# Performance work log

Measured on AMD Instinct MI355X. Metric: run time of the kernel, lower is better.

The kernel has to match this reference:

```python
import jax, jax.numpy as jnp
import numpy as np

B, C, Dz, Hh, Ww = 1, 128, 24, 24, 24
L = Dz * Hh * Ww
D_STATE = 16
D_CONV = 4
EXPAND = 2
D_INNER = EXPAND * C
DT_RANK = (C + 15) // 16  # ceil(d_model/16) = 8


def setup_inputs() -> dict:
    key = jax.random.key(0)
    ks = jax.random.split(key, 10)
    s = 0.02
    return {
        "x": jax.random.normal(ks[0], (B, C, Dz, Hh, Ww), dtype=jnp.float32),
        "ln_w": jnp.ones((C,), jnp.float32),
        "ln_b": jnp.zeros((C,), jnp.float32),
        "in_proj_w": s * jax.random.normal(ks[1], (2 * D_INNER, C), jnp.float32),
        "conv_w": s * jax.random.normal(ks[2], (D_INNER, D_CONV), jnp.float32),
        "conv_b": jnp.zeros((D_INNER,), jnp.float32),
        "x_proj_w": s * jax.random.normal(ks[3], (DT_RANK + 2 * D_STATE, D_INNER), jnp.float32),
        "dt_proj_w": s * jax.random.normal(ks[4], (D_INNER, DT_RANK), jnp.float32),
        "dt_proj_b": jax.random.uniform(ks[5], (D_INNER,), jnp.float32, -4.0, -2.0),
        "A_log": jnp.log(jnp.broadcast_to(jnp.arange(1, D_STATE + 1, dtype=jnp.float32), (D_INNER, D_STATE))),
        "D_param": jnp.ones((D_INNER,), jnp.float32),
        "out_proj_w": s * jax.random.normal(ks[6], (C, D_INNER), jnp.float32),
    }


def _mamba_forward(x, ln_w, ln_b, in_proj_w, conv_w, conv_b, x_proj_w,
                   dt_proj_w, dt_proj_b, A_log, D_param, out_proj_w):
    b, c, d, h, w = x.shape
    l = d * h * w
    tokens = x.reshape(b, c, l).transpose(0, 2, 1)  # (B,L,C)

    # LayerNorm over channel dim
    mu = jnp.mean(tokens, axis=-1, keepdims=True)
    var = jnp.var(tokens, axis=-1, keepdims=True)
    tn = (tokens - mu) * jax.lax.rsqrt(var + 1e-5) * ln_w + ln_b

    # in_proj -> x, z
    xz = jnp.einsum('blc,ec->ble', tn, in_proj_w)  # (B,L,2*d_inner)
    xs, z = jnp.split(xz, 2, axis=-1)

    # causal depthwise conv1d over L (kernel size D_CONV)
    xpad = jnp.pad(xs, ((0, 0), (D_CONV - 1, 0), (0, 0)))
    xc = conv_b
    xc = sum(xpad[:, k:k + l, :] * conv_w[:, k] for k in range(D_CONV)) + conv_b
    xa = jax.nn.silu(xc)  # (B,L,d_inner)

    # x_proj -> dt, B, C
    x_dbl = jnp.einsum('bld,ed->ble', xa, x_proj_w)
    dt_in = x_dbl[..., :DT_RANK]
    Bm = x_dbl[..., DT_RANK:DT_RANK + D_STATE]          # (B,L,d_state)
    Cm = x_dbl[..., DT_RANK + D_STATE:]                 # (B,L,d_state)
    dt = jax.nn.softplus(jnp.einsum('blr,dr->bld', dt_in, dt_proj_w) + dt_proj_b)

    A = -jnp.exp(A_log)  # (d_inner, d_state)

    def step(hst, inp):
        dt_t, B_t, C_t, x_t = inp  # (B,d_inner),(B,d_state),(B,d_state),(B,d_inner)
        dA = jnp.exp(dt_t[..., None] * A)                       # (B,d_inner,d_state)
        hst = dA * hst + (dt_t * x_t)[..., None] * B_t[:, None, :]
        y_t = jnp.einsum('bds,bs->bd', hst, C_t)
        return hst, y_t

    h0 = jnp.zeros((b, D_INNER, D_STATE), xa.dtype)
    xs_t = (dt.transpose(1, 0, 2), Bm.transpose(1, 0, 2), Cm.transpose(1, 0, 2), xa.transpose(1, 0, 2))
    _, ys = jax.lax.scan(step, h0, xs_t)
    y = ys.transpose(1, 0, 2) + xa * D_param  # (B,L,d_inner)

    y = y * jax.nn.silu(z)
    out = jnp.einsum('bld,cd->blc', y, out_proj_w)

    tokens = tokens + out
    return tokens.transpose(0, 2, 1).reshape(b, c, d, h, w)


def reference(x, ln_w, ln_b, in_proj_w, conv_w, conv_b, x_proj_w,
              dt_proj_w, dt_proj_b, A_log, D_param, out_proj_w):
    return _mamba_forward(x, ln_w, ln_b, in_proj_w, conv_w, conv_b, x_proj_w,
                          dt_proj_w, dt_proj_b, A_log, D_param, out_proj_w)
```

## Files before the change

kernel.cpp:

```cpp
#include <hip/hip_runtime.h>
#include <hip/hip_bf16.h>
#include <math.h>


constexpr int LQ = 13824;
constexpr int NC = 216;
constexpr int CH = 64;
constexpr int NB = 108;
constexpr int DI = 256;
constexpr int DS = 16;

typedef __attribute__((ext_vector_type(8))) short short8v;
typedef __attribute__((ext_vector_type(4))) float float4v;

__device__ __forceinline__ ushort f2bf(float f) {
  uint u = __float_as_uint(f);
  u += 0x7FFFu + ((u >> 16) & 1u);
  return (ushort)(u >> 16);
}
__device__ __forceinline__ float bf2f(ushort u) {
  return __uint_as_float(((uint)u) << 16);
}
__device__ __forceinline__ void gl_lds16(const ushort* g, ushort* l) {
  __builtin_amdgcn_global_load_lds(
      (const __attribute__((address_space(1))) void*)g,
      (__attribute__((address_space(3))) void*)l, 16, 0, 0);
}

template<int CTRL>
__device__ __forceinline__ float dpp_add(float x) {
  int y = __builtin_amdgcn_update_dpp(0, __float_as_int(x), CTRL, 0xF, 0xF, true);
  return x + __int_as_float(y);
}
__device__ __forceinline__ float quad_reduce(float t) {
  t = dpp_add<0xB1>(t);
  t = dpp_add<0x4E>(t);
  return t;
}
__device__ __forceinline__ float softplus_f(float x) {
  return (x > 20.f) ? x : log1pf(__expf(x));
}

__global__ __launch_bounds__(256) void prep_w2(const float* __restrict__ w_in,
    const float* __restrict__ w_xp, const float* __restrict__ w_dt,
    const float* __restrict__ w_out,
    ushort* __restrict__ b_in, ushort* __restrict__ b_xp2, ushort* __restrict__ b_out) {
  int idx = blockIdx.x * 256 + threadIdx.x;
  if (idx < 65536) {
    b_in[idx] = f2bf(w_in[idx]);
  } else if (idx < 65536 + 8192) {
    int j = idx - 65536; int r = j >> 8, k = j & 255;
    b_xp2[j] = f2bf(w_xp[(8 + r) * 256 + k]);
  } else if (idx < 65536 + 8192 + 65536) {
    int j = idx - (65536 + 8192); int d = j >> 8, k = j & 255;
    float acc = 0.f;
    #pragma unroll
    for (int r = 0; r < 8; ++r) acc += w_dt[d * 8 + r] * w_xp[r * 256 + k];
    b_xp2[8192 + j] = f2bf(acc);
  } else if (idx < 65536 + 8192 + 65536 + 8192) {
    b_xp2[73728 + (idx - 139264)] = 0;
  } else if (idx < 180224) {
    int j = idx - 147456;
    b_out[j] = f2bf(w_out[j]);
  }
}

__global__ __launch_bounds__(256) void ln_t(const float* __restrict__ x,
    const float* __restrict__ lnw, const float* __restrict__ lnb,
    ushort* __restrict__ tn) {
  __shared__ float red[64][8];
  __shared__ float stat[64][2];
  __shared__ ushort T[64][136];
  const int t = threadIdx.x;
  const int l = t & 63, q = t >> 6;
  const int l0 = blockIdx.x * 64;
  float sum = 0.f, sq = 0.f;
  #pragma unroll 8
  for (int cc = 0; cc < 32; ++cc) {
    int c = q * 32 + cc;
    float v = x[(size_t)c * LQ + l0 + l];
    sum += v; sq += v * v;
  }
  red[l][q] = sum; red[l][4 + q] = sq;
  __syncthreads();
  if (t < 64) {
    float s  = red[t][0] + red[t][1] + red[t][2] + red[t][3];
    float s2 = red[t][4] + red[t][5] + red[t][6] + red[t][7];
    float mu = s * (1.f / 128.f);
    float var = s2 * (1.f / 128.f) - mu * mu;
    stat[t][0] = mu; stat[t][1] = rsqrtf(var + 1e-5f);
  }
  __syncthreads();
  float mu = stat[l][0], rs = stat[l][1];
  #pragma unroll 8
  for (int cc = 0; cc < 32; ++cc) {
    int c = q * 32 + cc;
    float v = x[(size_t)c * LQ + l0 + l];
    T[l][c] = f2bf((v - mu) * rs * lnw[c] + lnb[c]);
  }
  __syncthreads();
  int row = t >> 2, seg = t & 3;
  #pragma unroll
  for (int j = 0; j < 4; ++j) {
    short8v v = *(const short8v*)&T[row][seg * 32 + j * 8];
    *(short8v*)&tn[(size_t)(l0 + row) * 128 + seg * 32 + j * 8] = v;
  }
}

template<int K, int MV, int BSTR, int CSTR>
__global__ __launch_bounds__(256) void gemm_tok(
    const ushort* __restrict__ Wb,
    const ushort* __restrict__ Act,
    ushort* __restrict__ Out) {
  constexpr int KO = K / 8;
  __shared__ ushort As[64 * K];
  __shared__ ushort Bs[2][128 * 64];
  const int tid = threadIdx.x;
  const int l0 = blockIdx.x * 128;
  const int m0 = blockIdx.y * 64;
  #pragma unroll
  for (int i = 0; i < (64 * KO) / 256; ++i) {
    int cid = i * 256 + tid;
    int m = cid / KO, oct = cid % KO;
    short8v v = *(const short8v*)&Wb[(size_t)(m0 + m) * K + oct * 8];
    *(short8v*)&As[m * K + ((oct ^ (m & 7)) * 8)] = v;
  }
  #pragma unroll
  for (int i = 0; i < 4; ++i) {
    int cid = i * 256 + tid;
    int l = cid >> 3, oct = (cid & 7) ^ (l & 7);
    gl_lds16(&Act[(size_t)(l0 + l) * BSTR + oct * 8], &Bs[0][cid * 8]);
  }
  float4v acc[4][2];
  #pragma unroll
  for (int a = 0; a < 4; ++a)
    #pragma unroll
    for (int b = 0; b < 2; ++b) acc[a][b] = (float4v)0.f;
  const int w = tid >> 6, lane = tid & 63;
  const int r = lane & 15, g = lane >> 4;
  int buf = 0;
  __syncthreads();
  for (int k0 = 0; k0 < K; k0 += 64) {
    if (k0 + 64 < K) {
      #pragma unroll
      for (int i = 0; i < 4; ++i) {
        int cid = i * 256 + tid;
        int l = cid >> 3, oct = (cid & 7) ^ (l & 7);
        gl_lds16(&Act[(size_t)(l0 + l) * BSTR + (k0 + 64) + oct * 8],
                 &Bs[buf ^ 1][cid * 8]);
      }
    }
    const ushort* bp = Bs[buf];
    #pragma unroll
    for (int kk = 0; kk < 2; ++kk) {
      short8v af[4], bfv[2];
      int ko = (k0 >> 3) + kk * 4 + g;
      #pragma unroll
      for (int mf = 0; mf < 4; ++mf) {
        int row = mf * 16 + r;
        af[mf] = *(const short8v*)&As[row * K + ((ko ^ (row & 7)) * 8)];
      }
      int kob = kk * 4 + g;
      #pragma unroll
      for (int nf = 0; nf < 2; ++nf) {
        int row = w * 32 + nf * 16 + r;
        bfv[nf] = *(const short8v*)&bp[row * 64 + ((kob ^ (row & 7)) * 8)];
      }
      #pragma unroll
      for (int mf = 0; mf < 4; ++mf)
        #pragma unroll
        for (int nf = 0; nf < 2; ++nf)
          acc[mf][nf] = __builtin_amdgcn_mfma_f32_16x16x32_bf16(af[mf], bfv[nf], acc[mf][nf], 0, 0, 0);
    }
    __syncthreads();
    buf ^= 1;
  }
  #pragma unroll
  for (int mf = 0; mf < 4; ++mf) {
    #pragma unroll
    for (int nf = 0; nf < 2; ++nf) {
      int l = w * 32 + nf * 16 + r;
      int m = mf * 16 + g * 4;
      ushort u0 = f2bf(acc[mf][nf][0]), u1 = f2bf(acc[mf][nf][1]);
      ushort u2 = f2bf(acc[mf][nf][2]), u3 = f2bf(acc[mf][nf][3]);
      uint2 pk = make_uint2((uint)u0 | ((uint)u1 << 16), (uint)u2 | ((uint)u3 << 16));
      int oct = (m >> 3) ^ (l & 7);
      *(uint2*)&Bs[0][l * 64 + oct * 8 + (g & 1) * 4] = pk;
    }
  }
  __syncthreads();
  #pragma unroll
  for (int i = 0; i < 4; ++i) {
    int cid = i * 256 + tid;
    int row = cid >> 3, oct = cid & 7;
    if (oct * 8 < MV) {
      short8v v = *(const short8v*)&Bs[0][row * 64 + ((oct ^ (row & 7)) * 8)];
      *(short8v*)&Out[(size_t)(l0 + row) * CSTR + m0 + oct * 8] = v;
    }
  }
}

__global__ __launch_bounds__(256) void gemm_out_k(
    const ushort* __restrict__ Wb,
    const ushort* __restrict__ Yg,
    const float* __restrict__ X,
    float* __restrict__ Out) {
  __shared__ ushort Ay[2][128 * 64];
  __shared__ ushort Bw[64 * 256];
  const int tid = threadIdx.x;
  const int l0 = blockIdx.x * 128;
  const int c0 = blockIdx.y * 64;
  const int w = tid >> 6, lane = tid & 63;
  const int r = lane & 15, g = lane >> 4;
  #pragma unroll
  for (int i = 0; i < 8; ++i) {
    int cid = i * 256 + tid;
    int row = cid >> 5, oct = cid & 31;
    short8v vb = *(const short8v*)&Wb[(size_t)(c0 + row) * 256 + oct * 8];
    *(short8v*)&Bw[row * 256 + ((oct ^ (row & 7)) * 8)] = vb;
  }
  #pragma unroll
  for (int i = 0; i < 4; ++i) {
    int cid = i * 256 + tid;
    int row = cid >> 3, oct = (cid & 7) ^ (row & 7);
    gl_lds16(&Yg[((size_t)(oct >> 1) * LQ + l0 + row) * 16 + (oct & 1) * 8],
             &Ay[0][cid * 8]);
  }
  float4v acc[2][4];
  #pragma unroll
  for (int a = 0; a < 2; ++a)
    #pragma unroll
    for (int b = 0; b < 4; ++b) acc[a][b] = (float4v)0.f;
  int buf = 0;
  __syncthreads();
  for (int k0 = 0; k0 < 256; k0 += 64) {
    if (k0 + 64 < 256) {
      int ks = (k0 + 64) >> 4;
      #pragma unroll
      for (int i = 0; i < 4; ++i) {
        int cid = i * 256 + tid;
        int row = cid >> 3, oct = (cid & 7) ^ (row & 7);
        gl_lds16(&Yg[((size_t)(ks + (oct >> 1)) * LQ + l0 + row) * 16 + (oct & 1) * 8],
                 &Ay[buf ^ 1][cid * 8]);
      }
    }
    const ushort* ap = Ay[buf];
    #pragma unroll
    for (int kk = 0; kk < 2; ++kk) {
      int kob = kk * 4 + g;
      int ko = (k0 >> 3) + kob;
      short8v af[2], bfv[4];
      #pragma unroll
      for (int mf = 0; mf < 2; ++mf) {
        int row = w * 32 + mf * 16 + r;
        af[mf] = *(const short8v*)&ap[row * 64 + ((kob ^ (row & 7)) * 8)];
      }
      #pragma unroll
      for (int nf = 0; nf < 4; ++nf) {
        int row = nf * 16 + r;
        bfv[nf] = *(const short8v*)&Bw[row * 256 + ((ko ^ (row & 7)) * 8)];
      }
      #pragma unroll
      for (int mf = 0; mf < 2; ++mf)
        #pragma unroll
        for (int nf = 0; nf < 4; ++nf)
          acc[mf][nf] = __builtin_amdgcn_mfma_f32_16x16x32_bf16(af[mf], bfv[nf], acc[mf][nf], 0, 0, 0);
    }
    __syncthreads();
    buf ^= 1;
  }
  #pragma unroll
  for (int mf = 0; mf < 2; ++mf) {
    #pragma unroll
    for (int nf = 0; nf < 4; ++nf) {
      int c = c0 + nf * 16 + r;
      int l = l0 + w * 32 + mf * 16 + g * 4;
      size_t off = (size_t)c * LQ + l;
      float4 rv = *(const float4*)&X[off];
      float4 o = make_float4(acc[mf][nf][0] + rv.x, acc[mf][nf][1] + rv.y,
                             acc[mf][nf][2] + rv.z, acc[mf][nf][3] + rv.w);
      *(float4*)&Out[off] = o;
    }
  }
}

__global__ __launch_bounds__(256) void conv2(const ushort* __restrict__ xz,
    const float* __restrict__ cw, const float* __restrict__ cb,
    ushort* __restrict__ xa) {
  const int tid = threadIdx.x;
  const int d0 = (tid & 31) * 8;
  const int l0 = blockIdx.x * 32 + (tid >> 5) * 4;
  float w0[8], w1[8], w2[8], w3[8], bb[8];
  #pragma unroll
  for (int j = 0; j < 8; ++j) {
    float4 wv = *(const float4*)&cw[(d0 + j) * 4];
    w0[j] = wv.x; w1[j] = wv.y; w2[j] = wv.z; w3[j] = wv.w;
    bb[j] = cb[d0 + j];
  }
  float rbuf[7][8];
  #pragma unroll
  for (int t = 0; t < 7; ++t) {
    int ls = l0 - 3 + t;
    if (ls >= 0) {
      short8v v = *(const short8v*)&xz[(size_t)ls * 512 + d0];
      #pragma unroll
      for (int j = 0; j < 8; ++j) rbuf[t][j] = bf2f((ushort)v[j]);
    } else {
      #pragma unroll
      for (int j = 0; j < 8; ++j) rbuf[t][j] = 0.f;
    }
  }
  #pragma unroll
  for (int i = 0; i < 4; ++i) {
    short8v ov;
    #pragma unroll
    for (int j = 0; j < 8; ++j) {
      float acc = bb[j] + w0[j] * rbuf[i][j] + w1[j] * rbuf[i + 1][j]
                        + w2[j] * rbuf[i + 2][j] + w3[j] * rbuf[i + 3][j];
      ov[j] = (short)f2bf(acc / (1.f + __expf(-acc)));
    }
    *(short8v*)&xa[(size_t)(l0 + i) * 256 + d0] = ov;
  }
}

__global__ __launch_bounds__(256) void scan1(const ushort* __restrict__ xdbl,
    const ushort* __restrict__ xa, const float* __restrict__ bias,
    const float* __restrict__ A_log, float* __restrict__ Stot, float* __restrict__ Hc,
    ushort* __restrict__ yloc) {
  __shared__ uint  duL[64 * 64];
  __shared__ float bcL[64 * 32];
  __shared__ ushort ylds[64 * 72];
  const int tid = threadIdx.x;
  const int c = blockIdx.x, dg = blockIdx.y;
  const int dloc = tid >> 2, sq = tid & 3;
  const int d = dg * 64 + dloc;
  const int lb = c * CH;
  float4v A, h;
  #pragma unroll
  for (int k = 0; k < 4; ++k) {
    A[k] = -__expf(A_log[d * 16 + sq * 4 + k]);
    h[k] = 0.f;
  }
  float S = 0.f;
  {
    const int doff = dg * 64 + sq * 16;
    const ushort* xr = xdbl + (size_t)(lb + dloc) * 320 + 32 + doff;
    const ushort* xar = xa + (size_t)(lb + dloc) * 256 + doff;
    short8v d0 = *(const short8v*)xr;
    short8v d1 = *(const short8v*)(xr + 8);
    short8v x0 = *(const short8v*)xar;
    short8v x1 = *(const short8v*)(xar + 8);
    uint pk[16];
    #pragma unroll
    for (int j = 0; j < 8; ++j) {
      float sp = softplus_f(bf2f((ushort)d0[j]) + bias[doff + j]);
      pk[j] = (uint)f2bf(sp) | ((uint)f2bf(sp * bf2f((ushort)x0[j])) << 16);
      float sp2 = softplus_f(bf2f((ushort)d1[j]) + bias[doff + 8 + j]);
      pk[8 + j] = (uint)f2bf(sp2) | ((uint)f2bf(sp2 * bf2f((ushort)x1[j])) << 16);
    }
    uint4* dst = (uint4*)&duL[dloc * 64 + sq * 16];
    #pragma unroll
    for (int j = 0; j < 4; ++j)
      dst[j] = make_uint4(pk[4 * j], pk[4 * j + 1], pk[4 * j + 2], pk[4 * j + 3]);
  }
  if (tid < 128) {
    int row = tid >> 1, half = tid & 1;
    const ushort* xr = xdbl + (size_t)(lb + row) * 320;
    short8v bv = *(const short8v*)(xr + half * 8);
    short8v cv = *(const short8v*)(xr + 16 + half * 8);
    float* bd = &bcL[row * 32 + half * 8];
    float* cd = &bcL[row * 32 + 16 + half * 8];
    #pragma unroll
    for (int j = 0; j < 8; ++j) {
      bd[j] = bf2f((ushort)bv[j]);
      cd[j] = bf2f((ushort)cv[j]);
    }
  }
  __syncthreads();
  #pragma unroll 4
  for (int i = 0; i < CH; ++i) {
    uint pv = duL[i * 64 + dloc];
    float dtv = __uint_as_float(pv << 16);
    float dxv = __uint_as_float(pv & 0xffff0000u);
    S += dtv;
    float4v Bv = *(const float4v*)&bcL[i * 32 + sq * 4];
    float4v Cv = *(const float4v*)&bcL[i * 32 + 16 + sq * 4];
    float t = 0.f;
    #pragma unroll
    for (int k = 0; k < 4; ++k) {
      float a = __expf(dtv * A[k]);
      h[k] = fmaf(a, h[k], dxv * Bv[k]);
      t = fmaf(h[k], Cv[k], t);
    }
    t = quad_reduce(t);
    if (sq == 0) ylds[i * 72 + dloc] = f2bf(t);
  }
  __syncthreads();
  {
    int slab = tid >> 6, row = tid & 63;
    short8v v0 = *(const short8v*)&ylds[row * 72 + slab * 16];
    short8v v1 = *(const short8v*)&ylds[row * 72 + slab * 16 + 8];
    ushort* dst = &yloc[((size_t)(dg * 4 + slab) * LQ + lb + row) * 16];
    *(short8v*)dst = v0;
    *(short8v*)(dst + 8) = v1;
  }
  *(float4*)&Hc[(size_t)(c * 256 + d) * 16 + sq * 4] = make_float4(h[0], h[1], h[2], h[3]);
  if (sq == 0) Stot[c * 256 + d] = S;
}

__global__ __launch_bounds__(256) void scan_combine(const float* __restrict__ Stot,
    const float* __restrict__ Hc, const float* __restrict__ A_log,
    float* __restrict__ Hin) {
  int t = blockIdx.x * 256 + threadIdx.x;
  int d = t >> 4;
  float A = -__expf(A_log[t]);
  float h = 0.f;
  for (int cb = 0; cb < NC; cb += 8) {
    float a[8], b[8];
    #pragma unroll
    for (int j = 0; j < 8; ++j) {
      a[j] = Stot[(cb + j) * 256 + d];
      b[j] = Hc[(size_t)(cb + j) * 4096 + t];
    }
    #pragma unroll
    for (int j = 0; j < 8; ++j) {
      Hin[(size_t)(cb + j) * 4096 + t] = h;
      h = fmaf(__expf(A * a[j]), h, b[j]);
    }
  }
}

__global__ __launch_bounds__(256) void scan2(const ushort* __restrict__ xdbl,
    const ushort* __restrict__ xa, const ushort* __restrict__ xz,
    const float* __restrict__ bias, const float* __restrict__ A_log,
    const float* __restrict__ Dp, const float* __restrict__ Hin,
    ushort* __restrict__ yg) {
  __shared__ uint  dtp[32 * 64];
  __shared__ float cL[64 * 16];
  __shared__ float corr[64 * 68];
  const int tid = threadIdx.x;
  const int c = blockIdx.x, dg = blockIdx.y;
  const int dloc = tid >> 2, sq = tid & 3;
  const int d = dg * 64 + dloc;
  const int lb = c * CH;
  float4v A, hin;
  #pragma unroll
  for (int k = 0; k < 4; ++k) A[k] = -__expf(A_log[d * 16 + sq * 4 + k]);
  {
    float4 hv = *(const float4*)&Hin[(size_t)(c * 256 + d) * 16 + sq * 4];
    hin[0] = hv.x; hin[1] = hv.y; hin[2] = hv.z; hin[3] = hv.w;
  }
  float S = 0.f;
  {
    int rp = tid >> 3, seg = tid & 7;
    const int doff = dg * 64 + seg * 8;
    const ushort* xr0 = xdbl + (size_t)(lb + 2 * rp) * 320 + 32 + doff;
    short8v e0 = *(const short8v*)xr0;
    short8v e1 = *(const short8v*)(xr0 + 320);
    uint pk[8];
    #pragma unroll
    for (int j = 0; j < 8; ++j) {
      float spe = softplus_f(bf2f((ushort)e0[j]) + bias[doff + j]);
      float spo = softplus_f(bf2f((ushort)e1[j]) + bias[doff + j]);
      pk[j] = (uint)f2bf(spe) | ((uint)f2bf(spo) << 16);
    }
    uint4* dst = (uint4*)&dtp[rp * 64 + seg * 8];
    dst[0] = make_uint4(pk[0], pk[1], pk[2], pk[3]);
    dst[1] = make_uint4(pk[4], pk[5], pk[6], pk[7]);
  }
  if (tid < 128) {
    int row = tid >> 1, half = tid & 1;
    short8v cv = *(const short8v*)(xdbl + (size_t)(lb + row) * 320 + 16 + half * 8);
    float* cd = &cL[row * 16 + half * 8];
    #pragma unroll
    for (int j = 0; j < 8; ++j) cd[j] = bf2f((ushort)cv[j]);
  }
  __syncthreads();
  #pragma unroll 2
  for (int i2 = 0; i2 < CH / 2; ++i2) {
    uint pv = dtp[i2 * 64 + dloc];
    #pragma unroll
    for (int par = 0; par < 2; ++par) {
      float dtv = (par == 0) ? __uint_as_float(pv << 16)
                             : __uint_as_float(pv & 0xffff0000u);
      S += dtv;
      int i = i2 * 2 + par;
      float4v Cv = *(const float4v*)&cL[i * 16 + sq * 4];
      float t = 0.f;
      #pragma unroll
      for (int k = 0; k < 4; ++k)
        t = fmaf(__expf(A[k] * S), hin[k] * Cv[k], t);
      t = quad_reduce(t);
      if (sq == 0) corr[i * 68 + dloc] = t;
    }
  }
  __syncthreads();
  {
    int slab = tid >> 6, row = tid & 63;
    const int doff = dg * 64 + slab * 16;
    size_t sl = ((size_t)(dg * 4 + slab) * LQ + lb + row) * 16;
    short8v y0 = *(const short8v*)&yg[sl];
    short8v y1 = *(const short8v*)&yg[sl + 8];
    const ushort* xav = xa + (size_t)(lb + row) * 256 + doff;
    short8v x0 = *(const short8v*)xav;
    short8v x1 = *(const short8v*)(xav + 8);
    const ushort* zvp = xz + (size_t)(lb + row) * 512 + 256 + doff;
    short8v z0 = *(const short8v*)zvp;
    short8v z1 = *(const short8v*)(zvp + 8);
    float4 c0 = *(const float4*)&corr[row * 68 + slab * 16];
    float4 c1 = *(const float4*)&corr[row * 68 + slab * 16 + 4];
    float4 c2 = *(const float4*)&corr[row * 68 + slab * 16 + 8];
    float4 c3 = *(const float4*)&corr[row * 68 + slab * 16 + 12];
    float cr[16] = {c0.x, c0.y, c0.z, c0.w, c1.x, c1.y, c1.z, c1.w,
                    c2.x, c2.y, c2.z, c2.w, c3.x, c3.y, c3.z, c3.w};
    short8v o0, o1;
    #pragma unroll
    for (int j = 0; j < 8; ++j) {
      float v0 = bf2f((ushort)y0[j]) + cr[j] + bf2f((ushort)x0[j]) * Dp[doff + j];
      float zf0 = bf2f((ushort)z0[j]);
      o0[j] = (short)f2bf(v0 * (zf0 / (1.f + __expf(-zf0))));
      float v1 = bf2f((ushort)y1[j]) + cr[8 + j] + bf2f((ushort)x1[j]) * Dp[doff + 8 + j];
      float zf1 = bf2f((ushort)z1[j]);
      o1[j] = (short)f2bf(v1 * (zf1 / (1.f + __expf(-zf1))));
    }
    *(short8v*)&yg[sl] = o0;
    *(short8v*)&yg[sl + 8] = o1;
  }
}

extern "C" void kernel_launch(void* const* d_in, const int* in_sizes, int n_in,
                              void* d_out, int out_size, void* d_ws, size_t ws_size,
                              hipStream_t stream) {
  const float* x         = (const float*)d_in[0];
  const float* ln_w      = (const float*)d_in[1];
  const float* ln_b      = (const float*)d_in[2];
  const float* in_proj_w = (const float*)d_in[3];
  const float* conv_w    = (const float*)d_in[4];
  const float* conv_b    = (const float*)d_in[5];
  const float* x_proj_w  = (const float*)d_in[6];
  const float* dt_proj_w = (const float*)d_in[7];
  const float* dt_proj_b = (const float*)d_in[8];
  const float* A_log     = (const float*)d_in[9];
  const float* D_param   = (const float*)d_in[10];
  const float* out_proj_w= (const float*)d_in[11];
  float* out = (float*)d_out;

  char* ws = (char*)d_ws;
  ushort* wbf_in  = (ushort*)(ws + 0);
  ushort* wbf_xp2 = (ushort*)(ws + 131072);
  ushort* wbf_out = (ushort*)(ws + 294912);
  float*  Hin     = (float*)(ws + 360448);
  float*  Hc      = (float*)(ws + 3899392);
  float*  Stot    = (float*)(ws + 7438336);
  ushort* tn_t    = (ushort*)(ws + 7659520);
  ushort* xz_t    = (ushort*)(ws + 11198464);
  ushort* xa_t    = (ushort*)(ws + 25354240);
  ushort* xdbl_t  = (ushort*)(ws + 32432128);
  ushort* yg_t    = (ushort*)(ws + 41279488);

  prep_w2<<<704, 256, 0, stream>>>(in_proj_w, x_proj_w, dt_proj_w, out_proj_w,
                                   wbf_in, wbf_xp2, wbf_out);
  ln_t<<<LQ / 64, 256, 0, stream>>>(x, ln_w, ln_b, tn_t);
  gemm_tok<128, 64, 128, 512><<<dim3(NB, 8), 256, 0, stream>>>(wbf_in, tn_t, xz_t);
  conv2<<<LQ / 32, 256, 0, stream>>>(xz_t, conv_w, conv_b, xa_t);
  gemm_tok<256, 64, 256, 320><<<dim3(NB, 5), 256, 0, stream>>>(wbf_xp2, xa_t, xdbl_t);
  scan1<<<dim3(NC, 4), 256, 0, stream>>>(xdbl_t, xa_t, dt_proj_b, A_log, Stot, Hc, yg_t);
  scan_combine<<<16, 256, 0, stream>>>(Stot, Hc, A_log, Hin);
  scan2<<<dim3(NC, 4), 256, 0, stream>>>(xdbl_t, xa_t, xz_t, dt_proj_b, A_log,
                                         D_param, Hin, yg_t);
  gemm_out_k<<<dim3(NB, 2), 256, 0, stream>>>(wbf_out, yg_t, x, out);
}
```

Measured before the change: 201.2 us.

## Fuse chunked scan stages into one cooperative kernel with grid syncs

```diff
diff --git a/kernel.cpp b/kernel.cpp
--- a/kernel.cpp
+++ b/kernel.cpp
@@ -1,6 +1,9 @@
 #include <hip/hip_runtime.h>
 #include <hip/hip_bf16.h>
+#include <hip/hip_cooperative_groups.h>
 #include <math.h>
+
+namespace cg = cooperative_groups;
 
 
 constexpr int LQ = 13824;
@@ -74,11 +77,12 @@
   const int t = threadIdx.x;
   const int l = t & 63, q = t >> 6;
   const int l0 = blockIdx.x * 64;
+  float vals[32];
   float sum = 0.f, sq = 0.f;
   #pragma unroll 8
   for (int cc = 0; cc < 32; ++cc) {
-    int c = q * 32 + cc;
-    float v = x[(size_t)c * LQ + l0 + l];
+    float v = x[(size_t)(q * 32 + cc) * LQ + l0 + l];
+    vals[cc] = v;
     sum += v; sq += v * v;
   }
   red[l][q] = sum; red[l][4 + q] = sq;
@@ -95,8 +99,7 @@
   #pragma unroll 8
   for (int cc = 0; cc < 32; ++cc) {
     int c = q * 32 + cc;
-    float v = x[(size_t)c * LQ + l0 + l];
-    T[l][c] = f2bf((v - mu) * rs * lnw[c] + lnb[c]);
+    T[l][c] = f2bf((vals[cc] - mu) * rs * lnw[c] + lnb[c]);
   }
   __syncthreads();
   int row = t >> 2, seg = t & 3;
@@ -323,13 +326,15 @@
   }
 }
 
-__global__ __launch_bounds__(256) void scan1(const ushort* __restrict__ xdbl,
-    const ushort* __restrict__ xa, const float* __restrict__ bias,
-    const float* __restrict__ A_log, float* __restrict__ Stot, float* __restrict__ Hc,
-    ushort* __restrict__ yloc) {
+__global__ __launch_bounds__(256, 4) void scan_fused(const ushort* __restrict__ xdbl,
+    const ushort* __restrict__ xa, const ushort* __restrict__ xz,
+    const float* __restrict__ bias, const float* __restrict__ A_log,
+    const float* __restrict__ Dp, float* __restrict__ Stot, float* __restrict__ Hc,
+    float* __restrict__ Hin, ushort* __restrict__ yg) {
   __shared__ uint  duL[64 * 64];
   __shared__ float bcL[64 * 32];
   __shared__ ushort ylds[64 * 72];
+  cg::grid_group gridg = cg::this_grid();
   const int tid = threadIdx.x;
   const int c = blockIdx.x, dg = blockIdx.y;
   const int dloc = tid >> 2, sq = tid & 3;
@@ -395,103 +400,51 @@
     t = quad_reduce(t);
     if (sq == 0) ylds[i * 72 + dloc] = f2bf(t);
   }
-  __syncthreads();
-  {
-    int slab = tid >> 6, row = tid & 63;
-    short8v v0 = *(const short8v*)&ylds[row * 72 + slab * 16];
-    short8v v1 = *(const short8v*)&ylds[row * 72 + slab * 16 + 8];
-    ushort* dst = &yloc[((size_t)(dg * 4 + slab) * LQ + lb + row) * 16];
-    *(short8v*)dst = v0;
-    *(short8v*)(dst + 8) = v1;
-  }
   *(float4*)&Hc[(size_t)(c * 256 + d) * 16 + sq * 4] = make_float4(h[0], h[1], h[2], h[3]);
   if (sq == 0) Stot[c * 256 + d] = S;
-}
-
-__global__ __launch_bounds__(256) void scan_combine(const float* __restrict__ Stot,
-    const float* __restrict__ Hc, const float* __restrict__ A_log,
-    float* __restrict__ Hin) {
-  int t = blockIdx.x * 256 + threadIdx.x;
-  int d = t >> 4;
-  float A = -__expf(A_log[t]);
-  float h = 0.f;
-  for (int cb = 0; cb < NC; cb += 8) {
-    float a[8], b[8];
-    #pragma unroll
-    for (int j = 0; j < 8; ++j) {
-      a[j] = Stot[(cb + j) * 256 + d];
-      b[j] = Hc[(size_t)(cb + j) * 4096 + t];
-    }
-    #pragma unroll
-    for (int j = 0; j < 8; ++j) {
-      Hin[(size_t)(cb + j) * 4096 + t] = h;
-      h = fmaf(__expf(A * a[j]), h, b[j]);
-    }
-  }
-}
-
-__global__ __launch_bounds__(256) void scan2(const ushort* __restrict__ xdbl,
-    const ushort* __restrict__ xa, const ushort* __restrict__ xz,
-    const float* __restrict__ bias, const float* __restrict__ A_log,
-    const float* __restrict__ Dp, const float* __restrict__ Hin,
-    ushort* __restrict__ yg) {
-  __shared__ uint  dtp[32 * 64];
-  __shared__ float cL[64 * 16];
-  __shared__ float corr[64 * 68];
-  const int tid = threadIdx.x;
-  const int c = blockIdx.x, dg = blockIdx.y;
-  const int dloc = tid >> 2, sq = tid & 3;
-  const int d = dg * 64 + dloc;
-  const int lb = c * CH;
-  float4v A, hin;
-  #pragma unroll
-  for (int k = 0; k < 4; ++k) A[k] = -__expf(A_log[d * 16 + sq * 4 + k]);
+  __threadfence();
+  gridg.sync();
+  if (blockIdx.x < 4) {
+    int t = (blockIdx.x * 4 + dg) * 256 + tid;
+    int dd = t >> 4;
+    float Ac = -__expf(A_log[t]);
+    float hh = 0.f;
+    for (int cb = 0; cb < NC; cb += 8) {
+      float a[8], b[8];
+      #pragma unroll
+      for (int j = 0; j < 8; ++j) {
+        a[j] = Stot[(cb + j) * 256 + dd];
+        b[j] = Hc[(size_t)(cb + j) * 4096 + t];
+      }
+      #pragma unroll
+      for (int j = 0; j < 8; ++j) {
+        Hin[(size_t)(cb + j) * 4096 + t] = hh;
+        hh = fmaf(__expf(Ac * a[j]), hh, b[j]);
+      }
+    }
+  }
+  __threadfence();
+  gridg.sync();
+  float4v hin;
   {
     float4 hv = *(const float4*)&Hin[(size_t)(c * 256 + d) * 16 + sq * 4];
     hin[0] = hv.x; hin[1] = hv.y; hin[2] = hv.z; hin[3] = hv.w;
   }
-  float S = 0.f;
-  {
-    int rp = tid >> 3, seg = tid & 7;
-    const int doff = dg * 64 + seg * 8;
-    const ushort* xr0 = xdbl + (size_t)(lb + 2 * rp) * 320 + 32 + doff;
-    short8v e0 = *(const short8v*)xr0;
-    short8v e1 = *(const short8v*)(xr0 + 320);
-    uint pk[8];
-    #pragma unroll
-    for (int j = 0; j < 8; ++j) {
-      float spe = softplus_f(bf2f((ushort)e0[j]) + bias[doff + j]);
-      float spo = softplus_f(bf2f((ushort)e1[j]) + bias[doff + j]);
-      pk[j] = (uint)f2bf(spe) | ((uint)f2bf(spo) << 16);
-    }
-    uint4* dst = (uint4*)&dtp[rp * 64 + seg * 8];
-    dst[0] = make_uint4(pk[0], pk[1], pk[2], pk[3]);
-    dst[1] = make_uint4(pk[4], pk[5], pk[6], pk[7]);
-  }
-  if (tid < 128) {
-    int row = tid >> 1, half = tid & 1;
-    short8v cv = *(const short8v*)(xdbl + (size_t)(lb + row) * 320 + 16 + half * 8);
-    float* cd = &cL[row * 16 + half * 8];
-    #pragma unroll
-    for (int j = 0; j < 8; ++j) cd[j] = bf2f((ushort)cv[j]);
-  }
-  __syncthreads();
-  #pragma unroll 2
-  for (int i2 = 0; i2 < CH / 2; ++i2) {
-    uint pv = dtp[i2 * 64 + dloc];
-    #pragma unroll
-    for (int par = 0; par < 2; ++par) {
-      float dtv = (par == 0) ? __uint_as_float(pv << 16)
-                             : __uint_as_float(pv & 0xffff0000u);
-      S += dtv;
-      int i = i2 * 2 + par;
-      float4v Cv = *(const float4v*)&cL[i * 16 + sq * 4];
-      float t = 0.f;
-      #pragma unroll
-      for (int k = 0; k < 4; ++k)
-        t = fmaf(__expf(A[k] * S), hin[k] * Cv[k], t);
-      t = quad_reduce(t);
-      if (sq == 0) corr[i * 68 + dloc] = t;
+  float S2 = 0.f;
+  #pragma unroll 4
+  for (int i = 0; i < CH; ++i) {
+    uint pv = duL[i * 64 + dloc];
+    float dtv = __uint_as_float(pv << 16);
+    S2 += dtv;
+    float4v Cv = *(const float4v*)&bcL[i * 32 + 16 + sq * 4];
+    float t = 0.f;
+    #pragma unroll
+    for (int k = 0; k < 4; ++k)
+      t = fmaf(__expf(A[k] * S2), hin[k] * Cv[k], t);
+    t = quad_reduce(t);
+    if (sq == 0) {
+      int yi = i * 72 + dloc;
+      ylds[yi] = f2bf(bf2f(ylds[yi]) + t);
     }
   }
   __syncthreads();
@@ -499,27 +452,21 @@
     int slab = tid >> 6, row = tid & 63;
     const int doff = dg * 64 + slab * 16;
     size_t sl = ((size_t)(dg * 4 + slab) * LQ + lb + row) * 16;
-    short8v y0 = *(const short8v*)&yg[sl];
-    short8v y1 = *(const short8v*)&yg[sl + 8];
+    short8v y0 = *(const short8v*)&ylds[row * 72 + slab * 16];
+    short8v y1 = *(const short8v*)&ylds[row * 72 + slab * 16 + 8];
     const ushort* xav = xa + (size_t)(lb + row) * 256 + doff;
     short8v x0 = *(const short8v*)xav;
     short8v x1 = *(const short8v*)(xav + 8);
     const ushort* zvp = xz + (size_t)(lb + row) * 512 + 256 + doff;
     short8v z0 = *(const short8v*)zvp;
     short8v z1 = *(const short8v*)(zvp + 8);
-    float4 c0 = *(const float4*)&corr[row * 68 + slab * 16];
-    float4 c1 = *(const float4*)&corr[row * 68 + slab * 16 + 4];
-    float4 c2 = *(const float4*)&corr[row * 68 + slab * 16 + 8];
-    float4 c3 = *(const float4*)&corr[row * 68 + slab * 16 + 12];
-    float cr[16] = {c0.x, c0.y, c0.z, c0.w, c1.x, c1.y, c1.z, c1.w,
-                    c2.x, c2.y, c2.z, c2.w, c3.x, c3.y, c3.z, c3.w};
     short8v o0, o1;
     #pragma unroll
     for (int j = 0; j < 8; ++j) {
-      float v0 = bf2f((ushort)y0[j]) + cr[j] + bf2f((ushort)x0[j]) * Dp[doff + j];
+      float v0 = bf2f((ushort)y0[j]) + bf2f((ushort)x0[j]) * Dp[doff + j];
       float zf0 = bf2f((ushort)z0[j]);
       o0[j] = (short)f2bf(v0 * (zf0 / (1.f + __expf(-zf0))));
-      float v1 = bf2f((ushort)y1[j]) + cr[8 + j] + bf2f((ushort)x1[j]) * Dp[doff + 8 + j];
+      float v1 = bf2f((ushort)y1[j]) + bf2f((ushort)x1[j]) * Dp[doff + 8 + j];
       float zf1 = bf2f((ushort)z1[j]);
       o1[j] = (short)f2bf(v1 * (zf1 / (1.f + __expf(-zf1))));
     }
@@ -564,9 +511,12 @@
   gemm_tok<128, 64, 128, 512><<<dim3(NB, 8), 256, 0, stream>>>(wbf_in, tn_t, xz_t);
   conv2<<<LQ / 32, 256, 0, stream>>>(xz_t, conv_w, conv_b, xa_t);
   gemm_tok<256, 64, 256, 320><<<dim3(NB, 5), 256, 0, stream>>>(wbf_xp2, xa_t, xdbl_t);
-  scan1<<<dim3(NC, 4), 256, 0, stream>>>(xdbl_t, xa_t, dt_proj_b, A_log, Stot, Hc, yg_t);
-  scan_combine<<<16, 256, 0, stream>>>(Stot, Hc, A_log, Hin);
-  scan2<<<dim3(NC, 4), 256, 0, stream>>>(xdbl_t, xa_t, xz_t, dt_proj_b, A_log,
-                                         D_param, Hin, yg_t);
+  {
+    void* args[] = {(void*)&xdbl_t, (void*)&xa_t, (void*)&xz_t, (void*)&dt_proj_b,
+                    (void*)&A_log, (void*)&D_param, (void*)&Stot, (void*)&Hc,
+                    (void*)&Hin, (void*)&yg_t};
+    hipLaunchCooperativeKernel((void*)scan_fused, dim3(NC, 4), dim3(256),
+                               args, 0, stream);
+  }
   gemm_out_k<<<dim3(NB, 2), 256, 0, stream>>>(wbf_out, yg_t, x, out);
 }
```

Measured after the change: 487.9 us. +142.5%, slower.

## Fuse depthwise conv into in_proj GEMM and merge weight prep with LayerNorm

Applied to the files above, without the earlier changes.

```diff
diff --git a/kernel.cpp b/kernel.cpp
--- a/kernel.cpp
+++ b/kernel.cpp
@@ -41,69 +41,215 @@
   return (x > 20.f) ? x : log1pf(__expf(x));
 }
 
-__global__ __launch_bounds__(256) void prep_w2(const float* __restrict__ w_in,
+__global__ __launch_bounds__(256) void prep_ln(const float* __restrict__ w_in,
     const float* __restrict__ w_xp, const float* __restrict__ w_dt,
     const float* __restrict__ w_out,
-    ushort* __restrict__ b_in, ushort* __restrict__ b_xp2, ushort* __restrict__ b_out) {
-  int idx = blockIdx.x * 256 + threadIdx.x;
-  if (idx < 65536) {
-    b_in[idx] = f2bf(w_in[idx]);
-  } else if (idx < 65536 + 8192) {
-    int j = idx - 65536; int r = j >> 8, k = j & 255;
-    b_xp2[j] = f2bf(w_xp[(8 + r) * 256 + k]);
-  } else if (idx < 65536 + 8192 + 65536) {
-    int j = idx - (65536 + 8192); int d = j >> 8, k = j & 255;
+    const float* __restrict__ x, const float* __restrict__ lnw,
+    const float* __restrict__ lnb,
+    ushort* __restrict__ b_in, ushort* __restrict__ b_xp2, ushort* __restrict__ b_out,
+    ushort* __restrict__ tn) {
+  if (blockIdx.x < 704) {
+    int idx = blockIdx.x * 256 + threadIdx.x;
+    if (idx < 65536) {
+      b_in[idx] = f2bf(w_in[idx]);
+    } else if (idx < 65536 + 8192) {
+      int j = idx - 65536; int r = j >> 8, k = j & 255;
+      b_xp2[j] = f2bf(w_xp[(8 + r) * 256 + k]);
+    } else if (idx < 65536 + 8192 + 65536) {
+      int j = idx - (65536 + 8192); int d = j >> 8, k = j & 255;
+      float acc = 0.f;
+      #pragma unroll
+      for (int r = 0; r < 8; ++r) acc += w_dt[d * 8 + r] * w_xp[r * 256 + k];
+      b_xp2[8192 + j] = f2bf(acc);
+    } else if (idx < 65536 + 8192 + 65536 + 8192) {
+      b_xp2[73728 + (idx - 139264)] = 0;
+    } else if (idx < 180224) {
+      int j = idx - 147456;
+      b_out[j] = f2bf(w_out[j]);
+    }
+  } else {
+    __shared__ float red[64][8];
+    __shared__ float stat[64][2];
+    __shared__ ushort T[64][136];
+    const int t = threadIdx.x;
+    const int l = t & 63, q = t >> 6;
+    const int l0 = (blockIdx.x - 704) * 64;
+    float vals[32];
+    float sum = 0.f, sq = 0.f;
+    #pragma unroll 8
+    for (int cc = 0; cc < 32; ++cc) {
+      float v = x[(size_t)(q * 32 + cc) * LQ + l0 + l];
+      vals[cc] = v;
+      sum += v; sq += v * v;
+    }
+    red[l][q] = sum; red[l][4 + q] = sq;
+    __syncthreads();
+    if (t < 64) {
+      float s  = red[t][0] + red[t][1] + red[t][2] + red[t][3];
+      float s2 = red[t][4] + red[t][5] + red[t][6] + red[t][7];
+      float mu = s * (1.f / 128.f);
+      float var = s2 * (1.f / 128.f) - mu * mu;
+      stat[t][0] = mu; stat[t][1] = rsqrtf(var + 1e-5f);
+    }
+    __syncthreads();
+    float mu = stat[l][0], rs = stat[l][1];
+    #pragma unroll 8
+    for (int cc = 0; cc < 32; ++cc) {
+      int c = q * 32 + cc;
+      T[l][c] = f2bf((vals[cc] - mu) * rs * lnw[c] + lnb[c]);
+    }
+    __syncthreads();
+    int row = t >> 2, seg = t & 3;
+    #pragma unroll
+    for (int j = 0; j < 4; ++j) {
+      short8v v = *(const short8v*)&T[row][seg * 32 + j * 8];
+      *(short8v*)&tn[(size_t)(l0 + row) * 128 + seg * 32 + j * 8] = v;
+    }
+  }
+}
+
+__global__ __launch_bounds__(256) void gemm_in_conv(
+    const ushort* __restrict__ Wb,
+    const ushort* __restrict__ Act,
+    const float* __restrict__ cw, const float* __restrict__ cb,
+    ushort* __restrict__ xa, ushort* __restrict__ zt) {
+  constexpr int K = 128, KO = 16;
+  __shared__ ushort As[64 * K];
+  __shared__ ushort Bs[2][128 * 64];
+  __shared__ __align__(16) ushort bnd[3 * 64];
+  const int tid = threadIdx.x;
+  const int l0 = blockIdx.x * 128;
+  const int my = blockIdx.y;
+  const int m0 = my * 64;
+  const bool isconv = (my < 4);
+  #pragma unroll
+  for (int i = 0; i < 4; ++i) {
+    int cid = i * 256 + tid;
+    int m = cid / KO, oct = cid % KO;
+    short8v v = *(const short8v*)&Wb[(size_t)(m0 + m) * K + oct * 8];
+    *(short8v*)&As[m * K + ((oct ^ (m & 7)) * 8)] = v;
+  }
+  #pragma unroll
+  for (int i = 0; i < 4; ++i) {
+    int cid = i * 256 + tid;
+    int l = cid >> 3, oct = (cid & 7) ^ (l & 7);
+    gl_lds16(&Act[(size_t)(l0 + l) * 128 + oct * 8], &Bs[0][cid * 8]);
+  }
+  if (isconv && tid < 192) {
+    int r = tid >> 6, m = tid & 63;
+    int lg = l0 - 3 + r;
     float acc = 0.f;
-    #pragma unroll
-    for (int r = 0; r < 8; ++r) acc += w_dt[d * 8 + r] * w_xp[r * 256 + k];
-    b_xp2[8192 + j] = f2bf(acc);
-  } else if (idx < 65536 + 8192 + 65536 + 8192) {
-    b_xp2[73728 + (idx - 139264)] = 0;
-  } else if (idx < 180224) {
-    int j = idx - 147456;
-    b_out[j] = f2bf(w_out[j]);
-  }
-}
-
-__global__ __launch_bounds__(256) void ln_t(const float* __restrict__ x,
-    const float* __restrict__ lnw, const float* __restrict__ lnb,
-    ushort* __restrict__ tn) {
-  __shared__ float red[64][8];
-  __shared__ float stat[64][2];
-  __shared__ ushort T[64][136];
-  const int t = threadIdx.x;
-  const int l = t & 63, q = t >> 6;
-  const int l0 = blockIdx.x * 64;
-  float sum = 0.f, sq = 0.f;
-  #pragma unroll 8
-  for (int cc = 0; cc < 32; ++cc) {
-    int c = q * 32 + cc;
-    float v = x[(size_t)c * LQ + l0 + l];
-    sum += v; sq += v * v;
-  }
-  red[l][q] = sum; red[l][4 + q] = sq;
-  __syncthreads();
-  if (t < 64) {
-    float s  = red[t][0] + red[t][1] + red[t][2] + red[t][3];
-    float s2 = red[t][4] + red[t][5] + red[t][6] + red[t][7];
-    float mu = s * (1.f / 128.f);
-    float var = s2 * (1.f / 128.f) - mu * mu;
-    stat[t][0] = mu; stat[t][1] = rsqrtf(var + 1e-5f);
-  }
-  __syncthreads();
-  float mu = stat[l][0], rs = stat[l][1];
-  #pragma unroll 8
-  for (int cc = 0; cc < 32; ++cc) {
-    int c = q * 32 + cc;
-    float v = x[(size_t)c * LQ + l0 + l];
-    T[l][c] = f2bf((v - mu) * rs * lnw[c] + lnb[c]);
-  }
-  __syncthreads();
-  int row = t >> 2, seg = t & 3;
-  #pragma unroll
-  for (int j = 0; j < 4; ++j) {
-    short8v v = *(const short8v*)&T[row][seg * 32 + j * 8];
-    *(short8v*)&tn[(size_t)(l0 + row) * 128 + seg * 32 + j * 8] = v;
+    if (lg >= 0) {
+      const ushort* wr = &Wb[(size_t)(m0 + m) * K];
+      const ushort* tr = &Act[(size_t)lg * 128];
+      for (int k = 0; k < 128; k += 8) {
+        short8v wv = *(const short8v*)&wr[k];
+        short8v tv = *(const short8v*)&tr[k];
+        #pragma unroll
+        for (int j = 0; j < 8; ++j)
+          acc = fmaf(bf2f((ushort)wv[j]), bf2f((ushort)tv[j]), acc);
+      }
+    }
+    bnd[r * 64 + m] = f2bf(acc);
+  }
+  float4v acc[4][2];
+  #pragma unroll
+  for (int a = 0; a < 4; ++a)
+    #pragma unroll
+    for (int b = 0; b < 2; ++b) acc[a][b] = (float4v)0.f;
+  const int w = tid >> 6, lane = tid & 63;
+  const int r = lane & 15, g = lane >> 4;
+  int buf = 0;
+  __syncthreads();
+  for (int k0 = 0; k0 < K; k0 += 64) {
+    if (k0 + 64 < K) {
+      #pragma unroll
+      for (int i = 0; i < 4; ++i) {
+        int cid = i * 256 + tid;
+        int l = cid >> 3, oct = (cid & 7) ^ (l & 7);
+        gl_lds16(&Act[(size_t)(l0 + l) * 128 + (k0 + 64) + oct * 8],
+                 &Bs[buf ^ 1][cid * 8]);
+      }
+    }
+    const ushort* bp = Bs[buf];
+    #pragma unroll
+    for (int kk = 0; kk < 2; ++kk) {
+      short8v af[4], bfv[2];
+      int ko = (k0 >> 3) + kk * 4 + g;
+      #pragma unroll
+      for (int mf = 0; mf < 4; ++mf) {
+        int row = mf * 16 + r;
+        af[mf] = *(const short8v*)&As[row * K + ((ko ^ (row & 7)) * 8)];
+      }
+      int kob = kk * 4 + g;
+      #pragma unroll
+      for (int nf = 0; nf < 2; ++nf) {
+        int row = w * 32 + nf * 16 + r;
+        bfv[nf] = *(const short8v*)&bp[row * 64 + ((kob ^ (row & 7)) * 8)];
+      }
+      #pragma unroll
+      for (int mf = 0; mf < 4; ++mf)
+        #pragma unroll
+        for (int nf = 0; nf < 2; ++nf)
+          acc[mf][nf] = __builtin_amdgcn_mfma_f32_16x16x32_bf16(af[mf], bfv[nf], acc[mf][nf], 0, 0, 0);
+    }
+    __syncthreads();
+    buf ^= 1;
+  }
+  #pragma unroll
+  for (int mf = 0; mf < 4; ++mf) {
+    #pragma unroll
+    for (int nf = 0; nf < 2; ++nf) {
+      int l = w * 32 + nf * 16 + r;
+      int m = mf * 16 + g * 4;
+      ushort u0 = f2bf(acc[mf][nf][0]), u1 = f2bf(acc[mf][nf][1]);
+      ushort u2 = f2bf(acc[mf][nf][2]), u3 = f2bf(acc[mf][nf][3]);
+      uint2 pk = make_uint2((uint)u0 | ((uint)u1 << 16), (uint)u2 | ((uint)u3 << 16));
+      int oct = (m >> 3) ^ (l & 7);
+      *(uint2*)&Bs[0][l * 64 + oct * 8 + (g & 1) * 4] = pk;
+    }
+  }
+  __syncthreads();
+  if (isconv) {
+    const int oct_ = tid & 7;
+    const int dbase = m0 + oct_ * 8;
+    float w0[8], w1[8], w2[8], w3[8], bb8[8];
+    #pragma unroll
+    for (int j = 0; j < 8; ++j) {
+      float4 wv = *(const float4*)&cw[(dbase + j) * 4];
+      w0[j] = wv.x; w1[j] = wv.y; w2[j] = wv.z; w3[j] = wv.w;
+      bb8[j] = cb[dbase + j];
+    }
+    #pragma unroll
+    for (int i = 0; i < 4; ++i) {
+      int cid = i * 256 + tid;
+      int row = cid >> 3, oct = cid & 7;
+      short8v s[4];
+      #pragma unroll
+      for (int t = 0; t < 4; ++t) {
+        int rr = row - 3 + t;
+        if (rr >= 0)
+          s[t] = *(const short8v*)&Bs[0][rr * 64 + ((oct ^ (rr & 7)) * 8)];
+        else
+          s[t] = *(const short8v*)&bnd[(rr + 3) * 64 + oct * 8];
+      }
+      short8v ov;
+      #pragma unroll
+      for (int j = 0; j < 8; ++j) {
+        float a = bb8[j] + w0[j] * bf2f((ushort)s[0][j]) + w1[j] * bf2f((ushort)s[1][j])
+                         + w2[j] * bf2f((ushort)s[2][j]) + w3[j] * bf2f((ushort)s[3][j]);
+        ov[j] = (short)f2bf(a / (1.f + __expf(-a)));
+      }
+      *(short8v*)&xa[(size_t)(l0 + row) * 256 + m0 + oct * 8] = ov;
+    }
+  } else {
+    #pragma unroll
+    for (int i = 0; i < 4; ++i) {
+      int cid = i * 256 + tid;
+      int row = cid >> 3, oct = cid & 7;
+      short8v v = *(const short8v*)&Bs[0][row * 64 + ((oct ^ (row & 7)) * 8)];
+      *(short8v*)&zt[(size_t)(l0 + row) * 256 + (m0 - 256) + oct * 8] = v;
+    }
   }
 }
 
@@ -281,45 +427,6 @@
                              acc[mf][nf][2] + rv.z, acc[mf][nf][3] + rv.w);
       *(float4*)&Out[off] = o;
     }
-  }
-}
-
-__global__ __launch_bounds__(256) void conv2(const ushort* __restrict__ xz,
-    const float* __restrict__ cw, const float* __restrict__ cb,
-    ushort* __restrict__ xa) {
-  const int tid = threadIdx.x;
-  const int d0 = (tid & 31) * 8;
-  const int l0 = blockIdx.x * 32 + (tid >> 5) * 4;
-  float w0[8], w1[8], w2[8], w3[8], bb[8];
-  #pragma unroll
-  for (int j = 0; j < 8; ++j) {
-    float4 wv = *(const float4*)&cw[(d0 + j) * 4];
-    w0[j] = wv.x; w1[j] = wv.y; w2[j] = wv.z; w3[j] = wv.w;
-    bb[j] = cb[d0 + j];
-  }
-  float rbuf[7][8];
-  #pragma unroll
-  for (int t = 0; t < 7; ++t) {
-    int ls = l0 - 3 + t;
-    if (ls >= 0) {
-      short8v v = *(const short8v*)&xz[(size_t)ls * 512 + d0];
-      #pragma unroll
-      for (int j = 0; j < 8; ++j) rbuf[t][j] = bf2f((ushort)v[j]);
-    } else {
-      #pragma unroll
-      for (int j = 0; j < 8; ++j) rbuf[t][j] = 0.f;
-    }
-  }
-  #pragma unroll
-  for (int i = 0; i < 4; ++i) {
-    short8v ov;
-    #pragma unroll
-    for (int j = 0; j < 8; ++j) {
-      float acc = bb[j] + w0[j] * rbuf[i][j] + w1[j] * rbuf[i + 1][j]
-                        + w2[j] * rbuf[i + 2][j] + w3[j] * rbuf[i + 3][j];
-      ov[j] = (short)f2bf(acc / (1.f + __expf(-acc)));
-    }
-    *(short8v*)&xa[(size_t)(l0 + i) * 256 + d0] = ov;
   }
 }
 
@@ -431,7 +538,7 @@
 }
 
 __global__ __launch_bounds__(256) void scan2(const ushort* __restrict__ xdbl,
-    const ushort* __restrict__ xa, const ushort* __restrict__ xz,
+    const ushort* __restrict__ xa, const ushort* __restrict__ zt,
     const float* __restrict__ bias, const float* __restrict__ A_log,
     const float* __restrict__ Dp, const float* __restrict__ Hin,
     ushort* __restrict__ yg) {
@@ -504,7 +611,7 @@
     const ushort* xav = xa + (size_t)(lb + row) * 256 + doff;
     short8v x0 = *(const short8v*)xav;
     short8v x1 = *(const short8v*)(xav + 8);
-    const ushort* zvp = xz + (size_t)(lb + row) * 512 + 256 + doff;
+    const ushort* zvp = zt + (size_t)(lb + row) * 256 + doff;
     short8v z0 = *(const short8v*)zvp;
     short8v z1 = *(const short8v*)(zvp + 8);
     float4 c0 = *(const float4*)&corr[row * 68 + slab * 16];
@@ -553,20 +660,18 @@
   float*  Hc      = (float*)(ws + 3899392);
   float*  Stot    = (float*)(ws + 7438336);
   ushort* tn_t    = (ushort*)(ws + 7659520);
-  ushort* xz_t    = (ushort*)(ws + 11198464);
-  ushort* xa_t    = (ushort*)(ws + 25354240);
-  ushort* xdbl_t  = (ushort*)(ws + 32432128);
-  ushort* yg_t    = (ushort*)(ws + 41279488);
-
-  prep_w2<<<704, 256, 0, stream>>>(in_proj_w, x_proj_w, dt_proj_w, out_proj_w,
-                                   wbf_in, wbf_xp2, wbf_out);
-  ln_t<<<LQ / 64, 256, 0, stream>>>(x, ln_w, ln_b, tn_t);
-  gemm_tok<128, 64, 128, 512><<<dim3(NB, 8), 256, 0, stream>>>(wbf_in, tn_t, xz_t);
-  conv2<<<LQ / 32, 256, 0, stream>>>(xz_t, conv_w, conv_b, xa_t);
+  ushort* zt      = (ushort*)(ws + 11198464);
+  ushort* xa_t    = (ushort*)(ws + 18276352);
+  ushort* xdbl_t  = (ushort*)(ws + 25354240);
+  ushort* yg_t    = (ushort*)(ws + 34201600);
+
+  prep_ln<<<920, 256, 0, stream>>>(in_proj_w, x_proj_w, dt_proj_w, out_proj_w,
+                                   x, ln_w, ln_b, wbf_in, wbf_xp2, wbf_out, tn_t);
+  gemm_in_conv<<<dim3(NB, 8), 256, 0, stream>>>(wbf_in, tn_t, conv_w, conv_b, xa_t, zt);
   gemm_tok<256, 64, 256, 320><<<dim3(NB, 5), 256, 0, stream>>>(wbf_xp2, xa_t, xdbl_t);
   scan1<<<dim3(NC, 4), 256, 0, stream>>>(xdbl_t, xa_t, dt_proj_b, A_log, Stot, Hc, yg_t);
   scan_combine<<<16, 256, 0, stream>>>(Stot, Hc, A_log, Hin);
-  scan2<<<dim3(NC, 4), 256, 0, stream>>>(xdbl_t, xa_t, xz_t, dt_proj_b, A_log,
+  scan2<<<dim3(NC, 4), 256, 0, stream>>>(xdbl_t, xa_t, zt, dt_proj_b, A_log,
                                          D_param, Hin, yg_t);
   gemm_out_k<<<dim3(NB, 2), 256, 0, stream>>>(wbf_out, yg_t, x, out);
 }
```

Result: no change. 203.0 us (+0.9%).
